# Optimization experiments

Hardware: AMD Instinct MI355X
Metric: run time of the kernel (lower is better)

Reference implementation:

```python
import jax, jax.numpy as jnp
import numpy as np

N_NODES = 50000


def setup_inputs() -> dict:
    key = jax.random.key(0)
    k1, k2, k3, k4, k5 = jax.random.split(key, 5)
    x = jax.random.normal(k1, (N_NODES, 128), dtype=jnp.float32)
    edge_index = jax.random.randint(k2, (2, 800000), 0, N_NODES, dtype=jnp.int64)
    # Linear layers: torch Linear stores weight as [out, in]; init ~ U(-1/sqrt(in), 1/sqrt(in))
    s = 1.0 / np.sqrt(128.0)
    W_rel = jax.random.uniform(k3, (128, 128), dtype=jnp.float32, minval=-s, maxval=s)
    b_rel = jax.random.uniform(k4, (128,), dtype=jnp.float32, minval=-s, maxval=s)
    W_root = jax.random.uniform(k5, (128, 128), dtype=jnp.float32, minval=-s, maxval=s)
    return {"x": x, "edge_index": edge_index, "W_rel": W_rel, "b_rel": b_rel, "W_root": W_root}


def reference(x, edge_index, W_rel, b_rel, W_root):
    # GraphConv (PyG): out_i = W_rel @ (sum_{j -> i} x_j) + b_rel + W_root @ x_i
    src, dst = edge_index[0], edge_index[1]
    msgs = x[src]  # [E, in] gather
    agg = jax.ops.segment_sum(msgs, dst, num_segments=N_NODES)  # [N, in] scatter-add
    out = agg @ W_rel.T + b_rel + x @ W_root.T
    # ReLU; dropout_rate = DropoutRate.NONE -> p=0, identity
    return jax.nn.relu(out)
```

## Files before the change

### kernel.cpp

```cpp
#include <hip/hip_runtime.h>
#include <hip/hip_bf16.h>
#include <hip/hip_cooperative_groups.h>

namespace cg = cooperative_groups;


#define F 128
#define NPB 32
#define NPARTS 8
#define CAP 128
#define CAPB 768
#define AST 68

typedef __bf16 bf16x8 __attribute__((ext_vector_type(8)));
typedef float f32x4 __attribute__((ext_vector_type(4)));

__device__ inline unsigned f32_to_bf16_rne(float f) {
  unsigned u = __float_as_uint(f);
  unsigned r = u + 0x7fffu + ((u >> 16) & 1u);
  return r >> 16;
}
__device__ inline unsigned pack2(float2 v) {
  return f32_to_bf16_rne(v.x) | (f32_to_bf16_rne(v.y) << 16);
}
__device__ inline unsigned pack2f(float a, float b) {
  return f32_to_bf16_rne(a) | (f32_to_bf16_rne(b) << 16);
}
__device__ inline void upk(unsigned v, float& ax, float& ay) {
  ax += __uint_as_float(v << 16);
  ay += __uint_as_float(v & 0xffff0000u);
}
__device__ inline void upk4(uint4 v, float* a) {
  a[0] += __uint_as_float(v.x << 16);
  a[1] += __uint_as_float(v.x & 0xffff0000u);
  a[2] += __uint_as_float(v.y << 16);
  a[3] += __uint_as_float(v.y & 0xffff0000u);
  a[4] += __uint_as_float(v.z << 16);
  a[5] += __uint_as_float(v.z & 0xffff0000u);
  a[6] += __uint_as_float(v.w << 16);
  a[7] += __uint_as_float(v.w & 0xffff0000u);
}

__global__ __launch_bounds__(256, 7) void mega_kernel(
    const float4* __restrict__ x, const float2* __restrict__ w0,
    const float2* __restrict__ w1, const int* __restrict__ ei,
    unsigned* __restrict__ xb, unsigned* __restrict__ wb,
    int* __restrict__ binCursor, unsigned* __restrict__ bin,
    const float* __restrict__ brel, float* __restrict__ out,
    int N, int E, int NB, int n4x, int n2w) {
  cg::grid_group grid = cg::this_grid();
  const int t = threadIdx.x;
  const int b = blockIdx.x;
  const int gtid = b * 256 + t;
  const int gstride = gridDim.x * 256;

  const int part = b & (NPARTS - 1);
  for (int e = gtid; e < E; e += gstride) {
    unsigned src = (unsigned)ei[e];
    unsigned dst = (unsigned)ei[E + e];
    int cell = part * NB + (int)(dst >> 5);
    int slot = atomicAdd(&binCursor[cell], 1);
    if (slot < CAP) bin[(size_t)cell * CAP + slot] = (dst << 16) | src;
  }
  uint2* __restrict__ xb2 = (uint2*)xb;
  for (int i = gtid; i < n4x; i += gstride) {
    float4 v = x[i];
    xb2[i] = make_uint2(pack2f(v.x, v.y), pack2f(v.z, v.w));
  }
  for (int i = gtid; i < 2 * n2w; i += gstride)
    wb[i] = (i < n2w) ? pack2(w0[i]) : pack2(w1[i - n2w]);
  grid.sync();

  __shared__ int cntS[NPB];
  __shared__ int offS[NPB];
  __shared__ int curS[NPB];
  __shared__ unsigned short eLds[CAPB];
  __shared__ unsigned aLds[NPB * AST];

  if (t < NPB) cntS[t] = 0;
  __syncthreads();

  unsigned kreg[NPARTS];
  int cnt_p[NPARTS];
#pragma unroll
  for (int p = 0; p < NPARTS; ++p) {
    int cell = p * NB + b;
    int c = min(binCursor[cell], CAP);
    cnt_p[p] = c;
    kreg[p] = (t < c) ? bin[(size_t)cell * CAP + t] : 0u;
  }
#pragma unroll
  for (int p = 0; p < NPARTS; ++p) {
    if (t < cnt_p[p]) atomicAdd(&cntS[(kreg[p] >> 16) & (NPB - 1)], 1);
  }
  __syncthreads();

  if (t < 64) {
    int v = (t < NPB) ? cntS[t] : 0;
    int incl = v;
#pragma unroll
    for (int off = 1; off < NPB; off <<= 1) {
      int u = __shfl_up(incl, off);
      if (t >= off) incl += u;
    }
    if (t < NPB) {
      offS[t] = incl - v;
      curS[t] = incl - v;
    }
  }
  __syncthreads();

#pragma unroll
  for (int p = 0; p < NPARTS; ++p) {
    if (t < cnt_p[p]) {
      int d = (kreg[p] >> 16) & (NPB - 1);
      int pos = atomicAdd(&curS[d], 1);
      if (pos < CAPB) eLds[pos] = (unsigned short)(kreg[p] & 0xffffu);
    }
  }
  __syncthreads();

  const int wave = t >> 6;
  const int lane = t & 63;
  const int grp = lane >> 4;
  const int l16 = lane & 15;
  const uint4* __restrict__ xb4 = (const uint4*)xb;
  const int nodeBase = b * NPB;
  for (int di = wave; di < NPB; di += 4) {
    float a8[8] = {0.f, 0.f, 0.f, 0.f, 0.f, 0.f, 0.f, 0.f};
    int beg = min(offS[di], CAPB);
    int end = min(offS[di] + cntS[di], CAPB);
    int e = beg;
    for (; e + 16 <= end; e += 16) {
      int s0 = eLds[e + grp];
      int s1 = eLds[e + 4 + grp];
      int s2 = eLds[e + 8 + grp];
      int s3 = eLds[e + 12 + grp];
      uint4 v0 = xb4[(size_t)s0 * 16 + l16];
      uint4 v1 = xb4[(size_t)s1 * 16 + l16];
      uint4 v2 = xb4[(size_t)s2 * 16 + l16];
      uint4 v3 = xb4[(size_t)s3 * 16 + l16];
      upk4(v0, a8);
      upk4(v1, a8);
      upk4(v2, a8);
      upk4(v3, a8);
    }
    if (e + 8 <= end) {
      int s0 = eLds[e + grp];
      int s1 = eLds[e + 4 + grp];
      uint4 v0 = xb4[(size_t)s0 * 16 + l16];
      uint4 v1 = xb4[(size_t)s1 * 16 + l16];
      upk4(v0, a8);
      upk4(v1, a8);
      e += 8;
    }
    if (e < end) {
      int i0 = e + grp;
      int i1 = e + 4 + grp;
      if (i0 < end) {
        uint4 v0 = xb4[(size_t)eLds[i0] * 16 + l16];
        upk4(v0, a8);
      }
      if (i1 < end) {
        uint4 v1 = xb4[(size_t)eLds[i1] * 16 + l16];
        upk4(v1, a8);
      }
    }
#pragma unroll
    for (int j = 0; j < 8; ++j) {
      a8[j] += __shfl_xor(a8[j], 16);
      a8[j] += __shfl_xor(a8[j], 32);
    }
    if (grp == 0) {
      uint4 pk;
      pk.x = pack2f(a8[0], a8[1]);
      pk.y = pack2f(a8[2], a8[3]);
      pk.z = pack2f(a8[4], a8[5]);
      pk.w = pack2f(a8[6], a8[7]);
      *((uint4*)&aLds[di * AST + l16 * 4]) = pk;
    }
  }
  __syncthreads();

  const int m16 = lane & 15;
  const int quad = lane >> 4;
  const f32x4 zero4 = {0.f, 0.f, 0.f, 0.f};
  const bf16x8 zero8 = {};
  f32x4 acc[2][2];
#pragma unroll
  for (int mt = 0; mt < 2; ++mt)
#pragma unroll
    for (int s = 0; s < 2; ++s) acc[mt][s] = zero4;

  const __bf16* __restrict__ wbb = (const __bf16*)wb;
#pragma unroll
  for (int ph = 0; ph < 2; ++ph) {
    const __bf16* __restrict__ W = wbb + (size_t)ph * F * F;
#pragma unroll
    for (int k0 = 0; k0 < F; k0 += 32) {
      const int kcol = k0 + 8 * quad;
      bf16x8 a[2], bw[2];
#pragma unroll
      for (int mt = 0; mt < 2; ++mt) {
        if (ph == 0) {
          a[mt] = *(const bf16x8*)&aLds[(mt * 16 + m16) * AST + (kcol >> 1)];
        } else {
          int row = nodeBase + mt * 16 + m16;
          a[mt] = (row < N)
                      ? *(const bf16x8*)((const __bf16*)xb + (size_t)row * F + kcol)
                      : zero8;
        }
      }
#pragma unroll
      for (int s = 0; s < 2; ++s) {
        int nt = wave * 2 + s;
        bw[s] = *(const bf16x8*)(W + (size_t)(nt * 16 + m16) * F + kcol);
      }
#pragma unroll
      for (int mt = 0; mt < 2; ++mt)
#pragma unroll
        for (int s = 0; s < 2; ++s)
          acc[mt][s] = __builtin_amdgcn_mfma_f32_16x16x32_bf16(
              a[mt], bw[s], acc[mt][s], 0, 0, 0);
    }
  }

#pragma unroll
  for (int s = 0; s < 2; ++s) {
    int nt = wave * 2 + s;
    float bias = brel[nt * 16 + m16];
#pragma unroll
    for (int mt = 0; mt < 2; ++mt) {
      int row0 = nodeBase + mt * 16 + quad * 4;
#pragma unroll
      for (int r = 0; r < 4; ++r) {
        int row = row0 + r;
        if (row < N)
          out[(size_t)row * F + nt * 16 + m16] = fmaxf(acc[mt][s][r] + bias, 0.f);
      }
    }
  }
}

__global__ __launch_bounds__(256) void prep_bin_kernel(
    const float2* __restrict__ x, const float2* __restrict__ w0,
    const float2* __restrict__ w1, const int* __restrict__ ei,
    unsigned* __restrict__ xb, unsigned* __restrict__ wb,
    int* __restrict__ binCursor, unsigned* __restrict__ bin,
    int E, int NB, int n2x, int n2w) {
  const int tid0 = blockIdx.x * blockDim.x + threadIdx.x;
  const int stride = gridDim.x * blockDim.x;
  const int totalc = n2x + 2 * n2w;
  for (int i = tid0; i < totalc; i += stride) {
    if (i < n2x) xb[i] = pack2(x[i]);
    else if (i < n2x + n2w) wb[i - n2x] = pack2(w0[i - n2x]);
    else wb[i - n2x] = pack2(w1[i - n2x - n2w]);
  }
  const int part = blockIdx.x & (NPARTS - 1);
  for (int e = tid0; e < E; e += stride) {
    unsigned src = (unsigned)ei[e];
    unsigned dst = (unsigned)ei[E + e];
    int cell = part * NB + (int)(dst >> 5);
    int slot = atomicAdd(&binCursor[cell], 1);
    if (slot < CAP) bin[(size_t)cell * CAP + slot] = (dst << 16) | src;
  }
}

__global__ __launch_bounds__(256) void agg_gemm_kernel(
    const unsigned* __restrict__ xb, const unsigned* __restrict__ bin,
    const int* __restrict__ binCursor, const __bf16* __restrict__ wb,
    const float* __restrict__ brel, float* __restrict__ out, int N, int NB) {
  __shared__ int cntS[NPB];
  __shared__ int offS[NPB];
  __shared__ int curS[NPB];
  __shared__ unsigned short eLds[CAPB];
  __shared__ unsigned aLds[NPB * AST];
  const int b = blockIdx.x;
  const int t = threadIdx.x;
  if (t < NPB) cntS[t] = 0;
  __syncthreads();
  unsigned kreg[NPARTS];
  int cnt_p[NPARTS];
#pragma unroll
  for (int p = 0; p < NPARTS; ++p) {
    int cell = p * NB + b;
    int c = min(binCursor[cell], CAP);
    cnt_p[p] = c;
    kreg[p] = (t < c) ? bin[(size_t)cell * CAP + t] : 0u;
  }
#pragma unroll
  for (int p = 0; p < NPARTS; ++p) {
    if (t < cnt_p[p]) atomicAdd(&cntS[(kreg[p] >> 16) & (NPB - 1)], 1);
  }
  __syncthreads();
  if (t < 64) {
    int v = (t < NPB) ? cntS[t] : 0;
    int incl = v;
#pragma unroll
    for (int off = 1; off < NPB; off <<= 1) {
      int u = __shfl_up(incl, off);
      if (t >= off) incl += u;
    }
    if (t < NPB) {
      offS[t] = incl - v;
      curS[t] = incl - v;
    }
  }
  __syncthreads();
#pragma unroll
  for (int p = 0; p < NPARTS; ++p) {
    if (t < cnt_p[p]) {
      int d = (kreg[p] >> 16) & (NPB - 1);
      int pos = atomicAdd(&curS[d], 1);
      if (pos < CAPB) eLds[pos] = (unsigned short)(kreg[p] & 0xffffu);
    }
  }
  __syncthreads();
  const int wave = t >> 6;
  const int lane = t & 63;
  const int nodeBase = b * NPB;
#pragma unroll
  for (int di = wave; di < NPB; di += 4) {
    float ax = 0.f, ay = 0.f;
    int beg = min(offS[di], CAPB);
    int end = min(offS[di] + cntS[di], CAPB);
    int e = beg;
    for (; e + 3 < end; e += 4) {
      int s0 = eLds[e + 0];
      int s1 = eLds[e + 1];
      int s2 = eLds[e + 2];
      int s3 = eLds[e + 3];
      unsigned v0 = xb[(size_t)s0 * 64 + lane];
      unsigned v1 = xb[(size_t)s1 * 64 + lane];
      unsigned v2 = xb[(size_t)s2 * 64 + lane];
      unsigned v3 = xb[(size_t)s3 * 64 + lane];
      upk(v0, ax, ay);
      upk(v1, ax, ay);
      upk(v2, ax, ay);
      upk(v3, ax, ay);
    }
    for (; e < end; ++e) upk(xb[(size_t)eLds[e] * 64 + lane], ax, ay);
    aLds[di * AST + lane] = f32_to_bf16_rne(ax) | (f32_to_bf16_rne(ay) << 16);
  }
  __syncthreads();
  const int m16 = lane & 15;
  const int quad = lane >> 4;
  const f32x4 zero4 = {0.f, 0.f, 0.f, 0.f};
  const bf16x8 zero8 = {};
  f32x4 acc[2][2];
#pragma unroll
  for (int mt = 0; mt < 2; ++mt)
#pragma unroll
    for (int s = 0; s < 2; ++s) acc[mt][s] = zero4;
#pragma unroll
  for (int ph = 0; ph < 2; ++ph) {
    const __bf16* __restrict__ W = wb + (size_t)ph * F * F;
#pragma unroll
    for (int k0 = 0; k0 < F; k0 += 32) {
      const int kcol = k0 + 8 * quad;
      bf16x8 a[2], bw[2];
#pragma unroll
      for (int mt = 0; mt < 2; ++mt) {
        if (ph == 0) {
          a[mt] = *(const bf16x8*)&aLds[(mt * 16 + m16) * AST + (kcol >> 1)];
        } else {
          int row = nodeBase + mt * 16 + m16;
          a[mt] = (row < N)
                      ? *(const bf16x8*)((const __bf16*)xb + (size_t)row * F + kcol)
                      : zero8;
        }
      }
#pragma unroll
      for (int s = 0; s < 2; ++s) {
        int nt = wave * 2 + s;
        bw[s] = *(const bf16x8*)(W + (size_t)(nt * 16 + m16) * F + kcol);
      }
#pragma unroll
      for (int mt = 0; mt < 2; ++mt)
#pragma unroll
        for (int s = 0; s < 2; ++s)
          acc[mt][s] = __builtin_amdgcn_mfma_f32_16x16x32_bf16(
              a[mt], bw[s], acc[mt][s], 0, 0, 0);
    }
  }
#pragma unroll
  for (int s = 0; s < 2; ++s) {
    int nt = wave * 2 + s;
    float bias = brel[nt * 16 + m16];
#pragma unroll
    for (int mt = 0; mt < 2; ++mt) {
      int row0 = nodeBase + mt * 16 + quad * 4;
#pragma unroll
      for (int r = 0; r < 4; ++r) {
        int row = row0 + r;
        if (row < N)
          out[(size_t)row * F + nt * 16 + m16] = fmaxf(acc[mt][s][r] + bias, 0.f);
      }
    }
  }
}

__global__ __launch_bounds__(256) void scatter_add_kernel(
    const float4* __restrict__ x4, const int* __restrict__ ei,
    float* __restrict__ agg, int E) {
  int gid = blockIdx.x * blockDim.x + threadIdx.x;
  if (gid >= E * 32) return;
  int e = gid >> 5, q = gid & 31;
  float4 v = x4[(size_t)ei[e] * 32 + q];
  float* a = agg + (size_t)ei[E + e] * F + q * 4;
  atomicAdd(a + 0, v.x);
  atomicAdd(a + 1, v.y);
  atomicAdd(a + 2, v.z);
  atomicAdd(a + 3, v.w);
}

#define ROWS_PER_BLOCK 64
#define SA_STRIDE 36
#define SW_STRIDE 132

__global__ __launch_bounds__(256) void gemm_fused_kernel(
    const float* __restrict__ agg, const float* __restrict__ x,
    const float* __restrict__ Wrel, const float* __restrict__ Wroot,
    const float* __restrict__ brel, float* __restrict__ out, int N) {
  __shared__ float sA[ROWS_PER_BLOCK * SA_STRIDE];
  __shared__ float sW[32 * SW_STRIDE];
  const int tid = threadIdx.x;
  const int j0 = (tid & 31) * 4;
  const int r0 = (tid >> 5) * 8;
  const int rowBase = blockIdx.x * ROWS_PER_BLOCK;
  float acc[8][4];
#pragma unroll
  for (int r = 0; r < 8; ++r)
#pragma unroll
    for (int c = 0; c < 4; ++c) acc[r][c] = 0.0f;
  for (int phase = 0; phase < 2; ++phase) {
    const float* __restrict__ A = phase ? x : agg;
    const float* __restrict__ W = phase ? Wroot : Wrel;
    for (int kc = 0; kc < F; kc += 32) {
#pragma unroll
      for (int idx = tid; idx < 512; idx += 256) {
        int row = idx >> 3, k4 = idx & 7;
        float4 v = make_float4(0.f, 0.f, 0.f, 0.f);
        int grow = rowBase + row;
        if (grow < N) v = *(const float4*)&A[(size_t)grow * F + kc + k4 * 4];
        *(float4*)&sA[row * SA_STRIDE + k4 * 4] = v;
      }
#pragma unroll
      for (int idx = tid; idx < 4096; idx += 256) {
        int j = idx >> 5, kk = idx & 31;
        sW[kk * SW_STRIDE + j] = W[j * F + kc + kk];
      }
      __syncthreads();
#pragma unroll
      for (int kk = 0; kk < 32; ++kk) {
        float4 w = *(const float4*)&sW[kk * SW_STRIDE + j0];
#pragma unroll
        for (int r = 0; r < 8; ++r) {
          float a = sA[(r0 + r) * SA_STRIDE + kk];
          acc[r][0] = fmaf(a, w.x, acc[r][0]);
          acc[r][1] = fmaf(a, w.y, acc[r][1]);
          acc[r][2] = fmaf(a, w.z, acc[r][2]);
          acc[r][3] = fmaf(a, w.w, acc[r][3]);
        }
      }
      __syncthreads();
    }
  }
  float b0 = brel[j0], b1 = brel[j0 + 1], b2 = brel[j0 + 2], b3 = brel[j0 + 3];
#pragma unroll
  for (int r = 0; r < 8; ++r) {
    int row = rowBase + r0 + r;
    if (row < N) {
      float4 v;
      v.x = fmaxf(acc[r][0] + b0, 0.0f);
      v.y = fmaxf(acc[r][1] + b1, 0.0f);
      v.z = fmaxf(acc[r][2] + b2, 0.0f);
      v.w = fmaxf(acc[r][3] + b3, 0.0f);
      *(float4*)&out[(size_t)row * F + j0] = v;
    }
  }
}

extern "C" void kernel_launch(void* const* d_in, const int* in_sizes, int n_in,
                              void* d_out, int out_size, void* d_ws, size_t ws_size,
                              hipStream_t stream) {
  const float* x     = (const float*)d_in[0];
  const int*   ei    = (const int*)d_in[1];
  const float* Wrel  = (const float*)d_in[2];
  const float* brel  = (const float*)d_in[3];
  const float* Wroot = (const float*)d_in[4];
  float* out = (float*)d_out;

  const int N = in_sizes[0] / F;
  const int E = in_sizes[1] / 2;
  const int NB = (N + NPB - 1) / NPB;

  size_t xbBytes  = ((size_t)N * F * 2 + 255) & ~(size_t)255;
  size_t wBytes   = ((size_t)2 * F * F * 2 + 255) & ~(size_t)255;
  size_t curBytes = ((size_t)NPARTS * NB * sizeof(int) + 255) & ~(size_t)255;
  size_t binBytes = ((size_t)NPARTS * NB * CAP * sizeof(unsigned) + 255) & ~(size_t)255;
  size_t needBin  = curBytes + binBytes + xbBytes + wBytes;

  if (ws_size >= needBin) {
    int*      binCursor = (int*)d_ws;
    unsigned* bin = (unsigned*)((char*)d_ws + curBytes);
    unsigned* xb  = (unsigned*)((char*)d_ws + curBytes + binBytes);
    unsigned* wb  = (unsigned*)((char*)d_ws + curBytes + binBytes + xbBytes);

    int n2x = N * (F / 2);
    int n4x = N * (F / 4);
    int n2w = F * F / 2;

    int maxBlocksPerCU = 0;
    hipError_t qerr = hipOccupancyMaxActiveBlocksPerMultiprocessor(
        &maxBlocksPerCU, (const void*)mega_kernel, 256, 0);
    bool coopOk = (qerr == hipSuccess) && (maxBlocksPerCU * 256 >= NB);

    if (coopOk) {
      hipMemsetAsync(binCursor, 0, (size_t)NPARTS * NB * sizeof(int), stream);
      const float4* xa = (const float4*)x;
      const float2* w0 = (const float2*)Wrel;
      const float2* w1 = (const float2*)Wroot;
      void* args[] = {(void*)&xa, (void*)&w0, (void*)&w1, (void*)&ei,
                      (void*)&xb, (void*)&wb, (void*)&binCursor, (void*)&bin,
                      (void*)&brel, (void*)&out,
                      (void*)&N, (void*)&E, (void*)&NB, (void*)&n4x, (void*)&n2w};
      hipError_t lerr = hipLaunchCooperativeKernel(
          (const void*)mega_kernel, dim3(NB), dim3(256), args, 0, stream);
      if (lerr == hipSuccess) return;
    }

    hipMemsetAsync(binCursor, 0, (size_t)NPARTS * NB * sizeof(int), stream);
    prep_bin_kernel<<<2048, 256, 0, stream>>>(
        (const float2*)x, (const float2*)Wrel, (const float2*)Wroot, ei, xb, wb,
        binCursor, bin, E, NB, n2x, n2w);
    agg_gemm_kernel<<<NB, 256, 0, stream>>>(xb, bin, binCursor,
                                            (const __bf16*)wb, brel, out, N, NB);
  } else {
    hipMemsetAsync(out, 0, (size_t)N * F * sizeof(float), stream);
    long long total = (long long)E * 32;
    scatter_add_kernel<<<(int)((total + 255) / 256), 256, 0, stream>>>(
        (const float4*)x, ei, out, E);
    gemm_fused_kernel<<<(N + ROWS_PER_BLOCK - 1) / ROWS_PER_BLOCK, 256, 0,
                        stream>>>(out, x, Wrel, Wroot, brel, out, N);
  }
}
```

Baseline: 171.6 us.

## Split cooperative mega-kernel into separate prep and aggregate-GEMM launches

Replaces the single cooperative-launch kernel, which used a grid-wide sync between edge binning/bf16 conversion and the aggregation+MFMA GEMM phase, with two ordinary kernel launches. The prep kernel runs on a fixed 2048-block grid. The agg/GEMM kernel keeps the mega-kernel's vectorized 8-wide aggregation path without the 7-blocks-per-CU launch bound. This removes the grid.sync cost and the occupancy constraint on the aggregation phase, in exchange for an extra kernel launch boundary.

```diff
diff --git a/kernel.cpp b/kernel.cpp
--- a/kernel.cpp
+++ b/kernel.cpp
@@ -1,8 +1,5 @@
 #include <hip/hip_runtime.h>
 #include <hip/hip_bf16.h>
-#include <hip/hip_cooperative_groups.h>
-
-namespace cg = cooperative_groups;
 
 
 #define F 128
@@ -25,10 +22,6 @@
 }
 __device__ inline unsigned pack2f(float a, float b) {
   return f32_to_bf16_rne(a) | (f32_to_bf16_rne(b) << 16);
-}
-__device__ inline void upk(unsigned v, float& ax, float& ay) {
-  ax += __uint_as_float(v << 16);
-  ay += __uint_as_float(v & 0xffff0000u);
 }
 __device__ inline void upk4(uint4 v, float* a) {
   a[0] += __uint_as_float(v.x << 16);
@@ -41,42 +34,43 @@
   a[7] += __uint_as_float(v.w & 0xffff0000u);
 }
 
-__global__ __launch_bounds__(256, 7) void mega_kernel(
+__global__ __launch_bounds__(256) void prep_bin2_kernel(
     const float4* __restrict__ x, const float2* __restrict__ w0,
     const float2* __restrict__ w1, const int* __restrict__ ei,
-    unsigned* __restrict__ xb, unsigned* __restrict__ wb,
+    uint2* __restrict__ xb2, unsigned* __restrict__ wb,
     int* __restrict__ binCursor, unsigned* __restrict__ bin,
-    const float* __restrict__ brel, float* __restrict__ out,
-    int N, int E, int NB, int n4x, int n2w) {
-  cg::grid_group grid = cg::this_grid();
-  const int t = threadIdx.x;
-  const int b = blockIdx.x;
-  const int gtid = b * 256 + t;
-  const int gstride = gridDim.x * 256;
-
-  const int part = b & (NPARTS - 1);
-  for (int e = gtid; e < E; e += gstride) {
+    int E, int NB, int n4x, int n2w) {
+  const int tid0 = blockIdx.x * 256 + threadIdx.x;
+  const int stride = gridDim.x * 256;
+
+  const int part = blockIdx.x & (NPARTS - 1);
+  for (int e = tid0; e < E; e += stride) {
     unsigned src = (unsigned)ei[e];
     unsigned dst = (unsigned)ei[E + e];
     int cell = part * NB + (int)(dst >> 5);
     int slot = atomicAdd(&binCursor[cell], 1);
     if (slot < CAP) bin[(size_t)cell * CAP + slot] = (dst << 16) | src;
   }
-  uint2* __restrict__ xb2 = (uint2*)xb;
-  for (int i = gtid; i < n4x; i += gstride) {
+  for (int i = tid0; i < n4x; i += stride) {
     float4 v = x[i];
     xb2[i] = make_uint2(pack2f(v.x, v.y), pack2f(v.z, v.w));
   }
-  for (int i = gtid; i < 2 * n2w; i += gstride)
+  for (int i = tid0; i < 2 * n2w; i += stride)
     wb[i] = (i < n2w) ? pack2(w0[i]) : pack2(w1[i - n2w]);
-  grid.sync();
-
+}
+
+__global__ __launch_bounds__(256) void agg_gemm2_kernel(
+    const unsigned* __restrict__ xb, const unsigned* __restrict__ bin,
+    const int* __restrict__ binCursor, const __bf16* __restrict__ wb,
+    const float* __restrict__ brel, float* __restrict__ out, int N, int NB) {
   __shared__ int cntS[NPB];
   __shared__ int offS[NPB];
   __shared__ int curS[NPB];
   __shared__ unsigned short eLds[CAPB];
   __shared__ unsigned aLds[NPB * AST];
 
+  const int b = blockIdx.x;
+  const int t = threadIdx.x;
   if (t < NPB) cntS[t] = 0;
   __syncthreads();
 
@@ -192,10 +186,9 @@
 #pragma unroll
     for (int s = 0; s < 2; ++s) acc[mt][s] = zero4;
 
-  const __bf16* __restrict__ wbb = (const __bf16*)wb;
 #pragma unroll
   for (int ph = 0; ph < 2; ++ph) {
-    const __bf16* __restrict__ W = wbb + (size_t)ph * F * F;
+    const __bf16* __restrict__ W = wb + (size_t)ph * F * F;
 #pragma unroll
     for (int k0 = 0; k0 < F; k0 += 32) {
       const int kcol = k0 + 8 * quad;
@@ -225,164 +218,6 @@
     }
   }
 
-#pragma unroll
-  for (int s = 0; s < 2; ++s) {
-    int nt = wave * 2 + s;
-    float bias = brel[nt * 16 + m16];
-#pragma unroll
-    for (int mt = 0; mt < 2; ++mt) {
-      int row0 = nodeBase + mt * 16 + quad * 4;
-#pragma unroll
-      for (int r = 0; r < 4; ++r) {
-        int row = row0 + r;
-        if (row < N)
-          out[(size_t)row * F + nt * 16 + m16] = fmaxf(acc[mt][s][r] + bias, 0.f);
-      }
-    }
-  }
-}
-
-__global__ __launch_bounds__(256) void prep_bin_kernel(
-    const float2* __restrict__ x, const float2* __restrict__ w0,
-    const float2* __restrict__ w1, const int* __restrict__ ei,
-    unsigned* __restrict__ xb, unsigned* __restrict__ wb,
-    int* __restrict__ binCursor, unsigned* __restrict__ bin,
-    int E, int NB, int n2x, int n2w) {
-  const int tid0 = blockIdx.x * blockDim.x + threadIdx.x;
-  const int stride = gridDim.x * blockDim.x;
-  const int totalc = n2x + 2 * n2w;
-  for (int i = tid0; i < totalc; i += stride) {
-    if (i < n2x) xb[i] = pack2(x[i]);
-    else if (i < n2x + n2w) wb[i - n2x] = pack2(w0[i - n2x]);
-    else wb[i - n2x] = pack2(w1[i - n2x - n2w]);
-  }
-  const int part = blockIdx.x & (NPARTS - 1);
-  for (int e = tid0; e < E; e += stride) {
-    unsigned src = (unsigned)ei[e];
-    unsigned dst = (unsigned)ei[E + e];
-    int cell = part * NB + (int)(dst >> 5);
-    int slot = atomicAdd(&binCursor[cell], 1);
-    if (slot < CAP) bin[(size_t)cell * CAP + slot] = (dst << 16) | src;
-  }
-}
-
-__global__ __launch_bounds__(256) void agg_gemm_kernel(
-    const unsigned* __restrict__ xb, const unsigned* __restrict__ bin,
-    const int* __restrict__ binCursor, const __bf16* __restrict__ wb,
-    const float* __restrict__ brel, float* __restrict__ out, int N, int NB) {
-  __shared__ int cntS[NPB];
-  __shared__ int offS[NPB];
-  __shared__ int curS[NPB];
-  __shared__ unsigned short eLds[CAPB];
-  __shared__ unsigned aLds[NPB * AST];
-  const int b = blockIdx.x;
-  const int t = threadIdx.x;
-  if (t < NPB) cntS[t] = 0;
-  __syncthreads();
-  unsigned kreg[NPARTS];
-  int cnt_p[NPARTS];
-#pragma unroll
-  for (int p = 0; p < NPARTS; ++p) {
-    int cell = p * NB + b;
-    int c = min(binCursor[cell], CAP);
-    cnt_p[p] = c;
-    kreg[p] = (t < c) ? bin[(size_t)cell * CAP + t] : 0u;
-  }
-#pragma unroll
-  for (int p = 0; p < NPARTS; ++p) {
-    if (t < cnt_p[p]) atomicAdd(&cntS[(kreg[p] >> 16) & (NPB - 1)], 1);
-  }
-  __syncthreads();
-  if (t < 64) {
-    int v = (t < NPB) ? cntS[t] : 0;
-    int incl = v;
-#pragma unroll
-    for (int off = 1; off < NPB; off <<= 1) {
-      int u = __shfl_up(incl, off);
-      if (t >= off) incl += u;
-    }
-    if (t < NPB) {
-      offS[t] = incl - v;
-      curS[t] = incl - v;
-    }
-  }
-  __syncthreads();
-#pragma unroll
-  for (int p = 0; p < NPARTS; ++p) {
-    if (t < cnt_p[p]) {
-      int d = (kreg[p] >> 16) & (NPB - 1);
-      int pos = atomicAdd(&curS[d], 1);
-      if (pos < CAPB) eLds[pos] = (unsigned short)(kreg[p] & 0xffffu);
-    }
-  }
-  __syncthreads();
-  const int wave = t >> 6;
-  const int lane = t & 63;
-  const int nodeBase = b * NPB;
-#pragma unroll
-  for (int di = wave; di < NPB; di += 4) {
-    float ax = 0.f, ay = 0.f;
-    int beg = min(offS[di], CAPB);
-    int end = min(offS[di] + cntS[di], CAPB);
-    int e = beg;
-    for (; e + 3 < end; e += 4) {
-      int s0 = eLds[e + 0];
-      int s1 = eLds[e + 1];
-      int s2 = eLds[e + 2];
-      int s3 = eLds[e + 3];
-      unsigned v0 = xb[(size_t)s0 * 64 + lane];
-      unsigned v1 = xb[(size_t)s1 * 64 + lane];
-      unsigned v2 = xb[(size_t)s2 * 64 + lane];
-      unsigned v3 = xb[(size_t)s3 * 64 + lane];
-      upk(v0, ax, ay);
-      upk(v1, ax, ay);
-      upk(v2, ax, ay);
-      upk(v3, ax, ay);
-    }
-    for (; e < end; ++e) upk(xb[(size_t)eLds[e] * 64 + lane], ax, ay);
-    aLds[di * AST + lane] = f32_to_bf16_rne(ax) | (f32_to_bf16_rne(ay) << 16);
-  }
-  __syncthreads();
-  const int m16 = lane & 15;
-  const int quad = lane >> 4;
-  const f32x4 zero4 = {0.f, 0.f, 0.f, 0.f};
-  const bf16x8 zero8 = {};
-  f32x4 acc[2][2];
-#pragma unroll
-  for (int mt = 0; mt < 2; ++mt)
-#pragma unroll
-    for (int s = 0; s < 2; ++s) acc[mt][s] = zero4;
-#pragma unroll
-  for (int ph = 0; ph < 2; ++ph) {
-    const __bf16* __restrict__ W = wb + (size_t)ph * F * F;
-#pragma unroll
-    for (int k0 = 0; k0 < F; k0 += 32) {
-      const int kcol = k0 + 8 * quad;
-      bf16x8 a[2], bw[2];
-#pragma unroll
-      for (int mt = 0; mt < 2; ++mt) {
-        if (ph == 0) {
-          a[mt] = *(const bf16x8*)&aLds[(mt * 16 + m16) * AST + (kcol >> 1)];
-        } else {
-          int row = nodeBase + mt * 16 + m16;
-          a[mt] = (row < N)
-                      ? *(const bf16x8*)((const __bf16*)xb + (size_t)row * F + kcol)
-                      : zero8;
-        }
-      }
-#pragma unroll
-      for (int s = 0; s < 2; ++s) {
-        int nt = wave * 2 + s;
-        bw[s] = *(const bf16x8*)(W + (size_t)(nt * 16 + m16) * F + kcol);
-      }
-#pragma unroll
-      for (int mt = 0; mt < 2; ++mt)
-#pragma unroll
-        for (int s = 0; s < 2; ++s)
-          acc[mt][s] = __builtin_amdgcn_mfma_f32_16x16x32_bf16(
-              a[mt], bw[s], acc[mt][s], 0, 0, 0);
-    }
-  }
 #pragma unroll
   for (int s = 0; s < 2; ++s) {
     int nt = wave * 2 + s;
@@ -507,35 +342,15 @@
     unsigned* xb  = (unsigned*)((char*)d_ws + curBytes + binBytes);
     unsigned* wb  = (unsigned*)((char*)d_ws + curBytes + binBytes + xbBytes);
 
-    int n2x = N * (F / 2);
     int n4x = N * (F / 4);
     int n2w = F * F / 2;
 
-    int maxBlocksPerCU = 0;
-    hipError_t qerr = hipOccupancyMaxActiveBlocksPerMultiprocessor(
-        &maxBlocksPerCU, (const void*)mega_kernel, 256, 0);
-    bool coopOk = (qerr == hipSuccess) && (maxBlocksPerCU * 256 >= NB);
-
-    if (coopOk) {
-      hipMemsetAsync(binCursor, 0, (size_t)NPARTS * NB * sizeof(int), stream);
-      const float4* xa = (const float4*)x;
-      const float2* w0 = (const float2*)Wrel;
-      const float2* w1 = (const float2*)Wroot;
-      void* args[] = {(void*)&xa, (void*)&w0, (void*)&w1, (void*)&ei,
-                      (void*)&xb, (void*)&wb, (void*)&binCursor, (void*)&bin,
-                      (void*)&brel, (void*)&out,
-                      (void*)&N, (void*)&E, (void*)&NB, (void*)&n4x, (void*)&n2w};
-      hipError_t lerr = hipLaunchCooperativeKernel(
-          (const void*)mega_kernel, dim3(NB), dim3(256), args, 0, stream);
-      if (lerr == hipSuccess) return;
-    }
-
     hipMemsetAsync(binCursor, 0, (size_t)NPARTS * NB * sizeof(int), stream);
-    prep_bin_kernel<<<2048, 256, 0, stream>>>(
-        (const float2*)x, (const float2*)Wrel, (const float2*)Wroot, ei, xb, wb,
-        binCursor, bin, E, NB, n2x, n2w);
-    agg_gemm_kernel<<<NB, 256, 0, stream>>>(xb, bin, binCursor,
-                                            (const __bf16*)wb, brel, out, N, NB);
+    prep_bin2_kernel<<<2048, 256, 0, stream>>>(
+        (const float4*)x, (const float2*)Wrel, (const float2*)Wroot, ei,
+        (uint2*)xb, wb, binCursor, bin, E, NB, n4x, n2w);
+    agg_gemm2_kernel<<<NB, 256, 0, stream>>>(xb, bin, binCursor,
+                                             (const __bf16*)wb, brel, out, N, NB);
   } else {
     hipMemsetAsync(out, 0, (size_t)N * F * sizeof(float), stream);
     long long total = (long long)E * 32;
```

New measurement: 167.7 us. 2.3% less time.
